# Kernel tuning notes

Measured on AMD Instinct MI355X. Metric: run time of the kernel, lower is better.

## Reference

```python
import jax, jax.numpy as jnp
import numpy as np

D_MODEL, D_STATE, D_CONV, EXPAND = 1024, 16, 4, 2
D_INNER = EXPAND * D_MODEL
BATCH, SEQ = 2, 2048


def setup_inputs() -> dict:
    key = jax.random.key(0)
    ks = jax.random.split(key, 10)
    s = lambda fan_in: 1.0 / np.sqrt(fan_in)
    return {
        "x": jax.random.normal(ks[0], (BATCH, SEQ, D_MODEL), jnp.float32),
        "W_in": jax.random.normal(ks[1], (2 * D_INNER, D_MODEL), jnp.float32) * s(D_MODEL),
        "w_conv": jax.random.normal(ks[2], (D_INNER, D_CONV), jnp.float32) * s(D_CONV),
        "b_conv": jax.random.normal(ks[3], (D_INNER,), jnp.float32) * 0.02,
        "W_x": jax.random.normal(ks[4], (D_INNER + 2 * D_STATE, D_INNER), jnp.float32) * s(D_INNER),
        "W_dt": jax.random.normal(ks[5], (D_INNER, D_INNER), jnp.float32) * s(D_INNER),
        "b_dt": jax.random.normal(ks[6], (D_INNER,), jnp.float32) * 0.02,
        "A_log": jnp.log(jax.random.uniform(ks[7], (D_INNER, D_STATE), jnp.float32, 1e-4, 1.0)),
        "D": jnp.ones((D_INNER,), jnp.float32),
        "W_out": jax.random.normal(ks[8], (D_MODEL, D_INNER), jnp.float32) * s(D_INNER),
    }


def _depthwise_causal_conv(x, w, b):
    # x: (B, L, C), w: (C, K), causal (left-pad K-1), matches conv1d(padding=K-1)[..., :L]
    K = w.shape[1]
    L = x.shape[1]
    xp = jnp.pad(x, ((0, 0), (K - 1, 0), (0, 0)))
    out = b
    for k in range(K):  # K is tiny (4)
        out = out + xp[:, k:k + L, :] * w[:, k]
    return out


def _selective_scan(x, delta, Bm, Cm, A, Dv):
    # x, delta: (B, L, d_inner); Bm, Cm: (B, L, d_state)
    def step(state, inp):
        x_t, d_t, B_t, C_t = inp  # (B,d_inner),(B,d_inner),(B,d_state),(B,d_state)
        decay = jnp.exp(d_t[..., None] * A)          # (B, d_inner, d_state)
        state = decay * state + B_t[:, None, :] * x_t[..., None]
        y_t = jnp.einsum('bds,bs->bd', state, C_t) + x_t * Dv
        return state, y_t

    init = jnp.zeros((x.shape[0], x.shape[2], A.shape[1]), x.dtype)
    xs = tuple(jnp.swapaxes(a, 0, 1) for a in (x, delta, Bm, Cm))
    _, ys = jax.lax.scan(step, init, xs)             # ys: (L, B, d_inner)
    return jnp.swapaxes(ys, 0, 1)


def reference(x, W_in, w_conv, b_conv, W_x, W_dt, b_dt, A_log, D, W_out):
    silu = jax.nn.silu
    xz = x @ W_in.T                                   # (B, L, 2*d_inner)
    x_inner, z = jnp.split(xz, 2, axis=-1)
    x_conv = silu(_depthwise_causal_conv(x_inner, w_conv, b_conv))
    x_dbl = x_conv @ W_x.T                            # (B, L, d_inner + 2*d_state)
    delta, Bm, Cm = jnp.split(x_dbl, [D_INNER, D_INNER + D_STATE], axis=-1)
    delta = jax.nn.softplus(delta @ W_dt.T + b_dt)
    A = -jnp.exp(A_log.astype(jnp.float32))
    y = _selective_scan(x_conv, delta, Bm, Cm, A, D)
    y = y * silu(z)
    return y @ W_out.T
```

## Files before the change

kernel.cpp:

```cpp
#include <hip/hip_runtime.h>
#include <hip/hip_bf16.h>


#define BATCH 2
#define SEQ   2048
#define DM    1024
#define DI    2048
#define DS    16
#define T_TOK (BATCH * SEQ)

#define CL 64
#define NC 32

typedef __bf16 v8bf __attribute__((ext_vector_type(8)));
typedef float  v4f  __attribute__((ext_vector_type(4)));

__device__ __forceinline__ void gld16(const void* g, void* l) {
    __builtin_amdgcn_global_load_lds(
        (const __attribute__((address_space(1))) void*)g,
        (__attribute__((address_space(3))) void*)l, 16, 0, 0);
}

__device__ __forceinline__ float b2f(__hip_bfloat16 v) { return __bfloat162float(v); }

__global__ void detect_dtype(const unsigned* __restrict__ Dptr, int* __restrict__ flag) {
    if (threadIdx.x == 0 && blockIdx.x == 0)
        *flag = (Dptr[0] == 0x3F803F80u) ? 1 : 0;
}

__device__ __forceinline__ float load_in(const void* p, size_t i, int isbf) {
    return isbf ? b2f(((const __hip_bfloat16*)p)[i]) : ((const float*)p)[i];
}

#define NBIG0 (T_TOK * DM)
#define NBIG1 (4096 * DM)
#define NBIG2 (DI * DI)
#define NBIG3 (DM * DI)
__global__ void convert_big(const void* __restrict__ s0, const void* __restrict__ s1,
                            const void* __restrict__ s2, const void* __restrict__ s3,
                            __hip_bfloat16* __restrict__ d0, __hip_bfloat16* __restrict__ d1,
                            __hip_bfloat16* __restrict__ d2, __hip_bfloat16* __restrict__ d3,
                            const int* __restrict__ flag) {
    if (*flag) return;
    size_t e = ((size_t)blockIdx.x * 256 + threadIdx.x) * 8;
    const float* src; __hip_bfloat16* dst;
    if (e < NBIG0)                      { src = (const float*)s0 + e;                 dst = d0 + e; }
    else if (e < NBIG0 + NBIG1)         { e -= NBIG0; src = (const float*)s1 + e;     dst = d1 + e; }
    else if (e < NBIG0 + NBIG1 + NBIG2) { e -= NBIG0 + NBIG1; src = (const float*)s2 + e; dst = d2 + e; }
    else                                { e -= NBIG0 + NBIG1 + NBIG2; src = (const float*)s3 + e; dst = d3 + e; }
    const float4 a = *(const float4*)src;
    const float4 b = *(const float4*)(src + 4);
    __bf16 o[8] = {(__bf16)a.x,(__bf16)a.y,(__bf16)a.z,(__bf16)a.w,
                   (__bf16)b.x,(__bf16)b.y,(__bf16)b.z,(__bf16)b.w};
    *(uint4*)dst = *(uint4*)&o[0];
}

__global__ void convert_small(const void* __restrict__ wconv, const void* __restrict__ bconv,
                              const void* __restrict__ bdt, const void* __restrict__ dv,
                              const void* __restrict__ A_log,
                              __hip_bfloat16* __restrict__ wconvb, __hip_bfloat16* __restrict__ bconvb,
                              __hip_bfloat16* __restrict__ bdtb, __hip_bfloat16* __restrict__ db,
                              float* __restrict__ Amat,
                              const int* __restrict__ flag) {
    const int isbf = *flag;
    const int i = blockIdx.x * 256 + threadIdx.x;
    if (i < 8192)        wconvb[i]        = __float2bfloat16(load_in(wconv, i, isbf));
    else if (i < 10240)  bconvb[i - 8192] = __float2bfloat16(load_in(bconv, i - 8192, isbf));
    else if (i < 12288)  bdtb[i - 10240]  = __float2bfloat16(load_in(bdt, i - 10240, isbf));
    else if (i < 14336)  db[i - 12288]    = __float2bfloat16(load_in(dv, i - 12288, isbf));
    else if (i < 47104)  Amat[i - 14336]  = -__expf(load_in(A_log, i - 14336, isbf));
}

__global__ __launch_bounds__(256) void transpose_wxd(
    const void* __restrict__ Wx, __hip_bfloat16* __restrict__ WxdT,
    const int* __restrict__ flag)
{
    const int isbf = *flag;
    __shared__ __bf16 t[64][72];
    const int bi = blockIdx.y * 64;
    const int bj = blockIdx.x * 64;
    const int rr = threadIdx.x >> 3;
    const int c0 = (threadIdx.x & 7) * 8;

#pragma unroll
    for (int k = 0; k < 2; k++) {
        const int r = rr + k * 32;
        const size_t src = (size_t)(bi + r) * DI + bj + c0;
        __bf16 o[8];
        if (isbf) {
            *(uint4*)&o[0] = *(const uint4*)((const __hip_bfloat16*)Wx + src);
        } else {
            const float* s = (const float*)Wx + src;
            const float4 a = *(const float4*)s;
            const float4 b = *(const float4*)(s + 4);
            o[0]=(__bf16)a.x; o[1]=(__bf16)a.y; o[2]=(__bf16)a.z; o[3]=(__bf16)a.w;
            o[4]=(__bf16)b.x; o[5]=(__bf16)b.y; o[6]=(__bf16)b.z; o[7]=(__bf16)b.w;
        }
        *(uint4*)&t[r][c0] = *(uint4*)&o[0];
    }
    __syncthreads();
#pragma unroll
    for (int k = 0; k < 2; k++) {
        const int dr = rr + k * 32;
        __bf16 o[8];
#pragma unroll
        for (int j = 0; j < 8; j++) o[j] = t[c0 + j][dr];
        *(uint4*)(WxdT + (size_t)(bj + dr) * DI + bi + c0) = *(uint4*)&o[0];
    }
}

__global__ void pad_bc(const void* __restrict__ Wx, __hip_bfloat16* __restrict__ Wxp,
                       const int* __restrict__ flag) {
    const int isbf = *flag;
    const size_t e = ((size_t)blockIdx.x * 256 + threadIdx.x) * 8;
    if (e >= (size_t)128 * DI) return;
    const size_t base = (size_t)2048 * DI;
    if (e >= (size_t)32 * DI) {
        __bf16 z[8] = {};
        *(uint4*)(Wxp + base + e) = *(uint4*)&z[0];
        return;
    }
    if (isbf) {
        *(uint4*)(Wxp + base + e) = *(const uint4*)((const __hip_bfloat16*)Wx + base + e);
    } else {
        const float* src = (const float*)Wx + base + e;
        const float4 a = *(const float4*)src;
        const float4 b = *(const float4*)(src + 4);
        __bf16 o[8] = {(__bf16)a.x,(__bf16)a.y,(__bf16)a.z,(__bf16)a.w,
                       (__bf16)b.x,(__bf16)b.y,(__bf16)b.z,(__bf16)b.w};
        *(uint4*)(Wxp + base + e) = *(uint4*)&o[0];
    }
}

template <int MODE, int TN>
__global__ __launch_bounds__(256) void gemm_bt(
    const __hip_bfloat16* __restrict__ Ac, const void* __restrict__ Araw,
    const __hip_bfloat16* __restrict__ Bc, const void* __restrict__ Braw,
    void* __restrict__ out0, void* __restrict__ out1,
    const __hip_bfloat16* __restrict__ bias,
    const int* __restrict__ flag,
    int M, int N, int K)
{
    constexpr int NF = TN / 32;
    constexpr int ASLOT = 512;
    constexpr int BSLOT = TN * 4;
    __shared__ v8bf Asv[2 * ASLOT];
    __shared__ v8bf Bsv[2 * BSLOT];

    const int isbf = *flag;
    const __hip_bfloat16* A  = (isbf && Araw) ? (const __hip_bfloat16*)Araw : Ac;
    const __hip_bfloat16* Bw = (isbf && Braw) ? (const __hip_bfloat16*)Braw : Bc;

    const int nx = gridDim.x;
    const int nblk = nx * gridDim.y;
    const int id = blockIdx.y * nx + blockIdx.x;
    const int sid = (id & 7) * (nblk >> 3) + (id >> 3);
    const int bxs = sid % nx;
    const int bys = sid / nx;

    const int tid  = threadIdx.x;
    const int bm   = bys * 128;
    const int bn   = bxs * TN;
    const int w    = tid >> 6;
    const int lane = tid & 63;
    const int wm   = (w >> 1) * 64;
    const int wn   = (w & 1) * (TN / 2);
    const int lrow  = lane & 15;
    const int lquad = lane >> 4;

    v4f acc[4][NF];
#pragma unroll
    for (int i = 0; i < 4; i++)
#pragma unroll
        for (int j = 0; j < NF; j++) acc[i][j] = (v4f){0.f, 0.f, 0.f, 0.f};

    const int r0 = tid >> 2;
    const int q0 = (tid & 3) ^ ((r0 >> 1) & 3);
    const __hip_bfloat16* gA0 = A  + (size_t)(bm + r0) * K + q0 * 8;
    const __hip_bfloat16* gA1 = A  + (size_t)(bm + 64 + r0) * K + q0 * 8;
    const __hip_bfloat16* gB0 = Bw + (size_t)(bn + r0) * K + q0 * 8;
    const __hip_bfloat16* gB1 = Bw + (size_t)(bn + 64 + r0) * K + q0 * 8;
    char* lA0 = (char*)Asv + tid * 16;
    char* lA1 = (char*)Asv + 4096 + tid * 16;
    char* lB0 = (char*)Bsv + tid * 16;
    char* lB1 = (char*)Bsv + 4096 + tid * 16;

    const int swz = lquad ^ ((lrow >> 1) & 3);
    int sA[4], sB[NF];
#pragma unroll
    for (int i = 0; i < 4; i++) sA[i] = (wm + i * 16 + lrow) * 4 + swz;
#pragma unroll
    for (int i = 0; i < NF; i++) sB[i] = (wn + i * 16 + lrow) * 4 + swz;

    const int NIT = K >> 5;
    gld16(gA0, lA0);
    gld16(gA1, lA1);
    gld16(gB0, lB0);
    if (TN == 128) gld16(gB1, lB1);

    int k = 32;
    for (int it = 0; it < NIT; ++it) {
        const int cb = it & 1;
        __syncthreads();
        if (it + 1 < NIT) {
            const int pa = (cb ^ 1) * 8192;
            const int pb = (cb ^ 1) * (BSLOT * 16);
            gld16(gA0 + k, lA0 + pa);
            gld16(gA1 + k, lA1 + pa);
            gld16(gB0 + k, lB0 + pb);
            if (TN == 128) gld16(gB1 + k, lB1 + pb);
            k += 32;
        }
        const int ca = cb * ASLOT;
        const int cbb = cb * BSLOT;
        v8bf af[4], bfr[NF];
#pragma unroll
        for (int i = 0; i < 4; i++)
            af[i] = Asv[ca + sA[i]];
#pragma unroll
        for (int i = 0; i < NF; i++)
            bfr[i] = Bsv[cbb + sB[i]];
#pragma unroll
        for (int mi = 0; mi < 4; mi++)
#pragma unroll
            for (int ni = 0; ni < NF; ni++)
                acc[mi][ni] = __builtin_amdgcn_mfma_f32_16x16x32_bf16(
                    af[mi], bfr[ni], acc[mi][ni], 0, 0, 0);
    }

#pragma unroll
    for (int mi = 0; mi < 4; mi++) {
#pragma unroll
        for (int ni = 0; ni < NF; ni++) {
#pragma unroll
            for (int r = 0; r < 4; r++) {
                const int grow = bm + wm + mi * 16 + lquad * 4 + r;
                const int gcol = bn + wn + ni * 16 + lrow;
                const float v = acc[mi][ni][r];
                if (MODE == 0) {
                    ((__hip_bfloat16*)out0)[(size_t)grow * N + gcol] = __float2bfloat16(v);
                } else if (MODE == 4) {
                    if (gcol < 2048) {
                        const float x = v + b2f(bias[gcol]);
                        const float sp = (x > 15.f) ? x : __logf(1.f + __expf(x));
                        ((__hip_bfloat16*)out0)[(size_t)grow * 2048 + gcol] = __float2bfloat16(sp);
                    } else if (gcol < 2080) {
                        ((float*)out1)[(size_t)grow * 32 + (gcol - 2048)] = v;
                    }
                } else {
                    if (isbf)
                        ((__hip_bfloat16*)out0)[(size_t)grow * N + gcol] = __float2bfloat16(v);
                    else
                        ((float*)out0)[(size_t)grow * N + gcol] = v;
                }
            }
        }
    }
}

__global__ __launch_bounds__(256) void conv_silu(
    const __hip_bfloat16* __restrict__ xz,
    const __hip_bfloat16* __restrict__ wconv,
    const __hip_bfloat16* __restrict__ bconv,
    __hip_bfloat16* __restrict__ xconv)
{
    const int idx = blockIdx.x * 256 + threadIdx.x;
    const int c8 = (idx & 255) << 3;
    const int tg = idx >> 8;
    const int tl = tg & (SEQ - 1);

    __bf16 wl[32], bl[8];
    *(uint4*)&wl[0]  = *(const uint4*)(wconv + c8 * 4);
    *(uint4*)&wl[8]  = *(const uint4*)(wconv + c8 * 4 + 8);
    *(uint4*)&wl[16] = *(const uint4*)(wconv + c8 * 4 + 16);
    *(uint4*)&wl[24] = *(const uint4*)(wconv + c8 * 4 + 24);
    *(uint4*)&bl[0]  = *(const uint4*)(bconv + c8);

    float acc[8];
#pragma unroll
    for (int cc = 0; cc < 8; cc++) acc[cc] = (float)bl[cc];

#pragma unroll
    for (int k = 0; k < 4; k++) {
        const int ts = tl - 3 + k;
        if (ts >= 0) {
            __bf16 xl[8];
            *(uint4*)&xl[0] = *(const uint4*)(xz + (size_t)(tg - 3 + k) * 4096 + c8);
#pragma unroll
            for (int cc = 0; cc < 8; cc++)
                acc[cc] += (float)wl[cc * 4 + k] * (float)xl[cc];
        }
    }

    __bf16 o[8];
#pragma unroll
    for (int cc = 0; cc < 8; cc++) {
        const float s = acc[cc] / (1.f + __expf(-acc[cc]));
        o[cc] = (__bf16)s;
    }
    *(uint4*)(xconv + (size_t)tg * DI + c8) = *(uint4*)&o[0];
}

__global__ __launch_bounds__(256) void scan_p1(
    const __hip_bfloat16* __restrict__ delta, const __hip_bfloat16* __restrict__ xconv,
    const float* __restrict__ BC, const float* __restrict__ Amat,
    float* __restrict__ Pws, float* __restrict__ Sws)
{
    const int d = blockIdx.x * 256 + threadIdx.x;
    const int c = blockIdx.y;
    const int b = blockIdx.z;
    const int tg0 = b * SEQ + c * CL;

    __shared__ float bc[CL * 32];
    for (int i = threadIdx.x; i < CL * 32; i += 256) bc[i] = BC[(size_t)tg0 * 32 + i];
    __syncthreads();

    float Areg[DS];
#pragma unroll
    for (int s = 0; s < DS; s++) Areg[s] = Amat[d * DS + s];

    float P[DS], S[DS];
#pragma unroll
    for (int s = 0; s < DS; s++) { P[s] = 1.f; S[s] = 0.f; }

    for (int i = 0; i < CL; i++) {
        const size_t tg = tg0 + i;
        const float dl = b2f(delta[tg * DI + d]);
        const float x  = b2f(xconv[tg * DI + d]);
#pragma unroll
        for (int s = 0; s < DS; s++) {
            const float e = __expf(dl * Areg[s]);
            P[s] *= e;
            S[s] = e * S[s] + bc[i * 32 + s] * x;
        }
    }

    const size_t base = (((size_t)b * NC + c) * DI + d) * DS;
#pragma unroll
    for (int s = 0; s < DS; s += 4) {
        *(float4*)(Pws + base + s) = make_float4(P[s], P[s+1], P[s+2], P[s+3]);
        *(float4*)(Sws + base + s) = make_float4(S[s], S[s+1], S[s+2], S[s+3]);
    }
}

__global__ void scan_p2(float* __restrict__ Pws, float* __restrict__ Sws) {
    const int idx = blockIdx.x * 256 + threadIdx.x;
    const int b  = idx >> 15;
    const int ds = idx & 32767;
    float carry = 0.f;
    for (int c = 0; c < NC; c++) {
        const size_t a = (((size_t)b * NC + c) << 15) + ds;
        const float p  = Pws[a];
        const float sv = Sws[a];
        Sws[a] = carry;
        carry = p * carry + sv;
    }
}

__global__ __launch_bounds__(256) void scan_p3(
    const __hip_bfloat16* __restrict__ delta, const __hip_bfloat16* __restrict__ xconv,
    const float* __restrict__ BC, const float* __restrict__ Amat,
    const float* __restrict__ Sws, const __hip_bfloat16* __restrict__ xz,
    const __hip_bfloat16* __restrict__ Dv, __hip_bfloat16* __restrict__ yg)
{
    const int d = blockIdx.x * 256 + threadIdx.x;
    const int c = blockIdx.y;
    const int b = blockIdx.z;
    const int tg0 = b * SEQ + c * CL;

    __shared__ float bc[CL * 32];
    for (int i = threadIdx.x; i < CL * 32; i += 256) bc[i] = BC[(size_t)tg0 * 32 + i];
    __syncthreads();

    float Areg[DS];
#pragma unroll
    for (int s = 0; s < DS; s++) Areg[s] = Amat[d * DS + s];

    const size_t base = (((size_t)b * NC + c) * DI + d) * DS;
    float S[DS];
#pragma unroll
    for (int s = 0; s < DS; s += 4) {
        const float4 v = *(const float4*)(Sws + base + s);
        S[s] = v.x; S[s+1] = v.y; S[s+2] = v.z; S[s+3] = v.w;
    }
    const float Dd = b2f(Dv[d]);

    for (int i = 0; i < CL; i++) {
        const size_t tg = tg0 + i;
        const float dl = b2f(delta[tg * DI + d]);
        const float x  = b2f(xconv[tg * DI + d]);
        float y = 0.f;
#pragma unroll
        for (int s = 0; s < DS; s++) {
            const float e = __expf(dl * Areg[s]);
            S[s] = e * S[s] + bc[i * 32 + s] * x;
            y += S[s] * bc[i * 32 + 16 + s];
        }
        y += x * Dd;
        const float z = b2f(xz[tg * 4096 + 2048 + d]);
        const float g = z / (1.f + __expf(-z));
        yg[tg * DI + d] = __float2bfloat16(y * g);
    }
}

extern "C" void kernel_launch(void* const* d_in, const int* in_sizes, int n_in,
                              void* d_out, int out_size, void* d_ws, size_t ws_size,
                              hipStream_t stream)
{
    const void* x_raw     = d_in[0];
    const void* W_in_raw  = d_in[1];
    const void* wconv_raw = d_in[2];
    const void* bconv_raw = d_in[3];
    const void* W_x_raw   = d_in[4];
    const void* W_dt_raw  = d_in[5];
    const void* b_dt_raw  = d_in[6];
    const void* A_log_raw = d_in[7];
    const void* D_raw     = d_in[8];
    const void* W_out_raw = d_in[9];

    char* ws = (char*)d_ws;
    size_t off = 0;
    auto alloc = [&](size_t bytes) { char* p = ws + off; off += (bytes + 255) & ~(size_t)255; return p; };
    int*            FLAG  = (int*)alloc(256);
    __hip_bfloat16* XB    = (__hip_bfloat16*)alloc((size_t)T_TOK * DM * 2);
    __hip_bfloat16* WINB  = (__hip_bfloat16*)alloc((size_t)4096 * DM * 2);
    __hip_bfloat16* WDTB  = (__hip_bfloat16*)alloc((size_t)DI * DI * 2);
    __hip_bfloat16* WOUTB = (__hip_bfloat16*)alloc((size_t)DM * DI * 2);
    __hip_bfloat16* WCONVB= (__hip_bfloat16*)alloc((size_t)DI * 4 * 2);
    __hip_bfloat16* BCONVB= (__hip_bfloat16*)alloc((size_t)DI * 2);
    __hip_bfloat16* BDTB  = (__hip_bfloat16*)alloc((size_t)DI * 2);
    __hip_bfloat16* DB    = (__hip_bfloat16*)alloc((size_t)DI * 2);
    __hip_bfloat16* XZ    = (__hip_bfloat16*)alloc((size_t)T_TOK * 4096 * 2);
    __hip_bfloat16* XCONV = (__hip_bfloat16*)alloc((size_t)T_TOK * DI * 2);
    __hip_bfloat16* WXDT  = (__hip_bfloat16*)alloc((size_t)DI * DI * 2);
    __hip_bfloat16* WXPAD = (__hip_bfloat16*)alloc((size_t)2176 * DI * 2);
    float*          BC    = (float*)alloc((size_t)T_TOK * 32 * 4);
    __hip_bfloat16* DELTA = (__hip_bfloat16*)alloc((size_t)T_TOK * DI * 2);
    float*          AMAT  = (float*)alloc((size_t)DI * DS * 4);
    float*          PWS   = (float*)alloc((size_t)BATCH * NC * DI * DS * 4);
    float*          SWS   = (float*)alloc((size_t)BATCH * NC * DI * DS * 4);
    __hip_bfloat16* YG    = (__hip_bfloat16*)alloc((size_t)T_TOK * DI * 2);

    detect_dtype<<<1, 64, 0, stream>>>((const unsigned*)D_raw, FLAG);
    convert_big<<<(NBIG0 + NBIG1 + NBIG2 + NBIG3) / (256 * 8), 256, 0, stream>>>(
        x_raw, W_in_raw, W_dt_raw, W_out_raw, XB, WINB, WDTB, WOUTB, FLAG);
    convert_small<<<184, 256, 0, stream>>>(wconv_raw, bconv_raw, b_dt_raw, D_raw, A_log_raw,
                                           WCONVB, BCONVB, BDTB, DB, AMAT, FLAG);
    transpose_wxd<<<dim3(32, 32), 256, 0, stream>>>(W_x_raw, WXDT, FLAG);

    gemm_bt<0, 128><<<dim3(16, 16), 256, 0, stream>>>(
        WDTB, W_dt_raw, WXDT, nullptr, WXPAD, nullptr, nullptr, FLAG, DI, DI, DI);

    pad_bc<<<128, 256, 0, stream>>>(W_x_raw, WXPAD, FLAG);

    gemm_bt<0, 128><<<dim3(32, 32), 256, 0, stream>>>(
        XB, x_raw, WINB, W_in_raw, XZ, nullptr, nullptr, FLAG, T_TOK, 4096, DM);

    conv_silu<<<T_TOK, 256, 0, stream>>>(XZ, WCONVB, BCONVB, XCONV);

    gemm_bt<4, 128><<<dim3(17, 32), 256, 0, stream>>>(
        XCONV, nullptr, WXPAD, nullptr, DELTA, BC, BDTB, FLAG, T_TOK, 2176, DI);

    scan_p1<<<dim3(DI / 256, NC, BATCH), 256, 0, stream>>>(DELTA, XCONV, BC, AMAT, PWS, SWS);
    scan_p2<<<(BATCH * DI * DS) / 256, 256, 0, stream>>>(PWS, SWS);
    scan_p3<<<dim3(DI / 256, NC, BATCH), 256, 0, stream>>>(DELTA, XCONV, BC, AMAT, SWS, XZ, DB, YG);

    gemm_bt<3, 64><<<dim3(16, 32), 256, 0, stream>>>(
        YG, nullptr, WOUTB, W_out_raw, d_out, nullptr, nullptr, FLAG, T_TOK, DM, DI);
}
```

Baseline: 468.6 us.

## Merge prep kernels, fuse dual GEMMs, grid-barrier scan, move softplus into scan

```diff
diff --git a/kernel.cpp b/kernel.cpp
--- a/kernel.cpp
+++ b/kernel.cpp
@@ -23,9 +23,8 @@
 
 __device__ __forceinline__ float b2f(__hip_bfloat16 v) { return __bfloat162float(v); }
 
-__global__ void detect_dtype(const unsigned* __restrict__ Dptr, int* __restrict__ flag) {
-    if (threadIdx.x == 0 && blockIdx.x == 0)
-        *flag = (Dptr[0] == 0x3F803F80u) ? 1 : 0;
+__device__ __forceinline__ int is_bf(const void* Dref) {
+    return ((const unsigned*)Dref)[0] == 0x3F803F80u;
 }
 
 __device__ __forceinline__ float load_in(const void* p, size_t i, int isbf) {
@@ -36,110 +35,110 @@
 #define NBIG1 (4096 * DM)
 #define NBIG2 (DI * DI)
 #define NBIG3 (DM * DI)
-__global__ void convert_big(const void* __restrict__ s0, const void* __restrict__ s1,
-                            const void* __restrict__ s2, const void* __restrict__ s3,
-                            __hip_bfloat16* __restrict__ d0, __hip_bfloat16* __restrict__ d1,
-                            __hip_bfloat16* __restrict__ d2, __hip_bfloat16* __restrict__ d3,
-                            const int* __restrict__ flag) {
-    if (*flag) return;
-    size_t e = ((size_t)blockIdx.x * 256 + threadIdx.x) * 8;
-    const float* src; __hip_bfloat16* dst;
-    if (e < NBIG0)                      { src = (const float*)s0 + e;                 dst = d0 + e; }
-    else if (e < NBIG0 + NBIG1)         { e -= NBIG0; src = (const float*)s1 + e;     dst = d1 + e; }
-    else if (e < NBIG0 + NBIG1 + NBIG2) { e -= NBIG0 + NBIG1; src = (const float*)s2 + e; dst = d2 + e; }
-    else                                { e -= NBIG0 + NBIG1 + NBIG2; src = (const float*)s3 + e; dst = d3 + e; }
-    const float4 a = *(const float4*)src;
-    const float4 b = *(const float4*)(src + 4);
-    __bf16 o[8] = {(__bf16)a.x,(__bf16)a.y,(__bf16)a.z,(__bf16)a.w,
-                   (__bf16)b.x,(__bf16)b.y,(__bf16)b.z,(__bf16)b.w};
-    *(uint4*)dst = *(uint4*)&o[0];
-}
-
-__global__ void convert_small(const void* __restrict__ wconv, const void* __restrict__ bconv,
-                              const void* __restrict__ bdt, const void* __restrict__ dv,
-                              const void* __restrict__ A_log,
-                              __hip_bfloat16* __restrict__ wconvb, __hip_bfloat16* __restrict__ bconvb,
-                              __hip_bfloat16* __restrict__ bdtb, __hip_bfloat16* __restrict__ db,
-                              float* __restrict__ Amat,
-                              const int* __restrict__ flag) {
-    const int isbf = *flag;
-    const int i = blockIdx.x * 256 + threadIdx.x;
-    if (i < 8192)        wconvb[i]        = __float2bfloat16(load_in(wconv, i, isbf));
-    else if (i < 10240)  bconvb[i - 8192] = __float2bfloat16(load_in(bconv, i - 8192, isbf));
-    else if (i < 12288)  bdtb[i - 10240]  = __float2bfloat16(load_in(bdt, i - 10240, isbf));
-    else if (i < 14336)  db[i - 12288]    = __float2bfloat16(load_in(dv, i - 12288, isbf));
-    else if (i < 47104)  Amat[i - 14336]  = -__expf(load_in(A_log, i - 14336, isbf));
-}
-
-__global__ __launch_bounds__(256) void transpose_wxd(
+#define NB_BIG 7168
+#define NB_TR  1024
+#define NB_SM  184
+#define NB_PAD 128
+#define NB_ALL (NB_BIG + NB_TR + NB_SM + NB_PAD)
+
+__global__ __launch_bounds__(256) void convert_all(
+    const void* __restrict__ s0, const void* __restrict__ s1,
+    const void* __restrict__ s2, const void* __restrict__ s3,
+    __hip_bfloat16* __restrict__ d0, __hip_bfloat16* __restrict__ d1,
+    __hip_bfloat16* __restrict__ d2, __hip_bfloat16* __restrict__ d3,
+    const void* __restrict__ wconv, const void* __restrict__ bconv,
+    const void* __restrict__ bdt, const void* __restrict__ dv,
+    const void* __restrict__ A_log,
+    __hip_bfloat16* __restrict__ wconvb, __hip_bfloat16* __restrict__ bconvb,
+    __hip_bfloat16* __restrict__ bdtb, __hip_bfloat16* __restrict__ db,
+    float* __restrict__ Amat,
     const void* __restrict__ Wx, __hip_bfloat16* __restrict__ WxdT,
-    const int* __restrict__ flag)
-{
-    const int isbf = *flag;
+    __hip_bfloat16* __restrict__ Wxp,
+    unsigned* __restrict__ bar)
+{
     __shared__ __bf16 t[64][72];
-    const int bi = blockIdx.y * 64;
-    const int bj = blockIdx.x * 64;
-    const int rr = threadIdx.x >> 3;
-    const int c0 = (threadIdx.x & 7) * 8;
-
-#pragma unroll
-    for (int k = 0; k < 2; k++) {
-        const int r = rr + k * 32;
-        const size_t src = (size_t)(bi + r) * DI + bj + c0;
-        __bf16 o[8];
-        if (isbf) {
-            *(uint4*)&o[0] = *(const uint4*)((const __hip_bfloat16*)Wx + src);
-        } else {
-            const float* s = (const float*)Wx + src;
-            const float4 a = *(const float4*)s;
-            const float4 b = *(const float4*)(s + 4);
-            o[0]=(__bf16)a.x; o[1]=(__bf16)a.y; o[2]=(__bf16)a.z; o[3]=(__bf16)a.w;
-            o[4]=(__bf16)b.x; o[5]=(__bf16)b.y; o[6]=(__bf16)b.z; o[7]=(__bf16)b.w;
-        }
-        *(uint4*)&t[r][c0] = *(uint4*)&o[0];
-    }
-    __syncthreads();
-#pragma unroll
-    for (int k = 0; k < 2; k++) {
-        const int dr = rr + k * 32;
-        __bf16 o[8];
-#pragma unroll
-        for (int j = 0; j < 8; j++) o[j] = t[c0 + j][dr];
-        *(uint4*)(WxdT + (size_t)(bj + dr) * DI + bi + c0) = *(uint4*)&o[0];
-    }
-}
-
-__global__ void pad_bc(const void* __restrict__ Wx, __hip_bfloat16* __restrict__ Wxp,
-                       const int* __restrict__ flag) {
-    const int isbf = *flag;
-    const size_t e = ((size_t)blockIdx.x * 256 + threadIdx.x) * 8;
-    if (e >= (size_t)128 * DI) return;
-    const size_t base = (size_t)2048 * DI;
-    if (e >= (size_t)32 * DI) {
-        __bf16 z[8] = {};
-        *(uint4*)(Wxp + base + e) = *(uint4*)&z[0];
-        return;
-    }
-    if (isbf) {
-        *(uint4*)(Wxp + base + e) = *(const uint4*)((const __hip_bfloat16*)Wx + base + e);
-    } else {
-        const float* src = (const float*)Wx + base + e;
+    const int isbf = is_bf(dv);
+    const int bid = blockIdx.x;
+
+    if (bid < NB_BIG) {
+        if (isbf) return;
+        size_t e = ((size_t)bid * 256 + threadIdx.x) * 8;
+        const float* src; __hip_bfloat16* dst;
+        if (e < NBIG0)                      { src = (const float*)s0 + e;                 dst = d0 + e; }
+        else if (e < NBIG0 + NBIG1)         { e -= NBIG0; src = (const float*)s1 + e;     dst = d1 + e; }
+        else if (e < NBIG0 + NBIG1 + NBIG2) { e -= NBIG0 + NBIG1; src = (const float*)s2 + e; dst = d2 + e; }
+        else                                { e -= NBIG0 + NBIG1 + NBIG2; src = (const float*)s3 + e; dst = d3 + e; }
         const float4 a = *(const float4*)src;
         const float4 b = *(const float4*)(src + 4);
         __bf16 o[8] = {(__bf16)a.x,(__bf16)a.y,(__bf16)a.z,(__bf16)a.w,
                        (__bf16)b.x,(__bf16)b.y,(__bf16)b.z,(__bf16)b.w};
-        *(uint4*)(Wxp + base + e) = *(uint4*)&o[0];
+        *(uint4*)dst = *(uint4*)&o[0];
+    } else if (bid < NB_BIG + NB_TR) {
+        const int b2 = bid - NB_BIG;
+        const int bi = (b2 >> 5) * 64;
+        const int bj = (b2 & 31) * 64;
+        const int rr = threadIdx.x >> 3;
+        const int c0 = (threadIdx.x & 7) * 8;
+#pragma unroll
+        for (int k = 0; k < 2; k++) {
+            const int r = rr + k * 32;
+            const size_t src = (size_t)(bi + r) * DI + bj + c0;
+            __bf16 o[8];
+            if (isbf) {
+                *(uint4*)&o[0] = *(const uint4*)((const __hip_bfloat16*)Wx + src);
+            } else {
+                const float* s = (const float*)Wx + src;
+                const float4 a = *(const float4*)s;
+                const float4 b = *(const float4*)(s + 4);
+                o[0]=(__bf16)a.x; o[1]=(__bf16)a.y; o[2]=(__bf16)a.z; o[3]=(__bf16)a.w;
+                o[4]=(__bf16)b.x; o[5]=(__bf16)b.y; o[6]=(__bf16)b.z; o[7]=(__bf16)b.w;
+            }
+            *(uint4*)&t[r][c0] = *(uint4*)&o[0];
+        }
+        __syncthreads();
+#pragma unroll
+        for (int k = 0; k < 2; k++) {
+            const int dr = rr + k * 32;
+            __bf16 o[8];
+#pragma unroll
+            for (int j = 0; j < 8; j++) o[j] = t[c0 + j][dr];
+            *(uint4*)(WxdT + (size_t)(bj + dr) * DI + bi + c0) = *(uint4*)&o[0];
+        }
+    } else if (bid < NB_BIG + NB_TR + NB_SM) {
+        if (bid == NB_BIG + NB_TR && threadIdx.x == 0) *bar = 0u;
+        const int i = (bid - (NB_BIG + NB_TR)) * 256 + threadIdx.x;
+        if (i < 8192)        wconvb[i]        = __float2bfloat16(load_in(wconv, i, isbf));
+        else if (i < 10240)  bconvb[i - 8192] = __float2bfloat16(load_in(bconv, i - 8192, isbf));
+        else if (i < 12288)  bdtb[i - 10240]  = __float2bfloat16(load_in(bdt, i - 10240, isbf));
+        else if (i < 14336)  db[i - 12288]    = __float2bfloat16(load_in(dv, i - 12288, isbf));
+        else if (i < 47104)  Amat[i - 14336]  = -__expf(load_in(A_log, i - 14336, isbf));
+    } else {
+        const size_t e = ((size_t)(bid - (NB_BIG + NB_TR + NB_SM)) * 256 + threadIdx.x) * 8;
+        if (e >= (size_t)128 * DI) return;
+        const size_t base = (size_t)2048 * DI;
+        if (e >= (size_t)32 * DI) {
+            __bf16 z[8] = {};
+            *(uint4*)(Wxp + base + e) = *(uint4*)&z[0];
+            return;
+        }
+        if (isbf) {
+            *(uint4*)(Wxp + base + e) = *(const uint4*)((const __hip_bfloat16*)Wx + base + e);
+        } else {
+            const float* src = (const float*)Wx + base + e;
+            const float4 a = *(const float4*)src;
+            const float4 b = *(const float4*)(src + 4);
+            __bf16 o[8] = {(__bf16)a.x,(__bf16)a.y,(__bf16)a.z,(__bf16)a.w,
+                           (__bf16)b.x,(__bf16)b.y,(__bf16)b.z,(__bf16)b.w};
+            *(uint4*)(Wxp + base + e) = *(uint4*)&o[0];
+        }
     }
 }
 
 template <int MODE, int TN>
-__global__ __launch_bounds__(256) void gemm_bt(
-    const __hip_bfloat16* __restrict__ Ac, const void* __restrict__ Araw,
-    const __hip_bfloat16* __restrict__ Bc, const void* __restrict__ Braw,
+__device__ __forceinline__ void gemm_core(
+    const __hip_bfloat16* __restrict__ A, const __hip_bfloat16* __restrict__ Bw,
     void* __restrict__ out0, void* __restrict__ out1,
-    const __hip_bfloat16* __restrict__ bias,
-    const int* __restrict__ flag,
-    int M, int N, int K)
+    int isbf, int id, int nx, int nblk, int N, int K)
 {
     constexpr int NF = TN / 32;
     constexpr int ASLOT = 512;
@@ -147,13 +146,6 @@
     __shared__ v8bf Asv[2 * ASLOT];
     __shared__ v8bf Bsv[2 * BSLOT];
 
-    const int isbf = *flag;
-    const __hip_bfloat16* A  = (isbf && Araw) ? (const __hip_bfloat16*)Araw : Ac;
-    const __hip_bfloat16* Bw = (isbf && Braw) ? (const __hip_bfloat16*)Braw : Bc;
-
-    const int nx = gridDim.x;
-    const int nblk = nx * gridDim.y;
-    const int id = blockIdx.y * nx + blockIdx.x;
     const int sid = (id & 7) * (nblk >> 3) + (id >> 3);
     const int bxs = sid % nx;
     const int bys = sid / nx;
@@ -239,11 +231,9 @@
                 const float v = acc[mi][ni][r];
                 if (MODE == 0) {
                     ((__hip_bfloat16*)out0)[(size_t)grow * N + gcol] = __float2bfloat16(v);
-                } else if (MODE == 4) {
+                } else if (MODE == 1) {
                     if (gcol < 2048) {
-                        const float x = v + b2f(bias[gcol]);
-                        const float sp = (x > 15.f) ? x : __logf(1.f + __expf(x));
-                        ((__hip_bfloat16*)out0)[(size_t)grow * 2048 + gcol] = __float2bfloat16(sp);
+                        ((__hip_bfloat16*)out0)[(size_t)grow * 2048 + gcol] = __float2bfloat16(v);
                     } else if (gcol < 2080) {
                         ((float*)out1)[(size_t)grow * 32 + (gcol - 2048)] = v;
                     }
@@ -258,6 +248,42 @@
     }
 }
 
+template <int MODE, int TN>
+__global__ __launch_bounds__(256) void gemm_single(
+    const __hip_bfloat16* __restrict__ Ac, const void* __restrict__ Araw,
+    const __hip_bfloat16* __restrict__ Bc, const void* __restrict__ Braw,
+    void* __restrict__ out0, void* __restrict__ out1,
+    const void* __restrict__ Dref, int N, int K)
+{
+    const int isbf = is_bf(Dref);
+    const __hip_bfloat16* A = (isbf && Araw) ? (const __hip_bfloat16*)Araw : Ac;
+    const __hip_bfloat16* B = (isbf && Braw) ? (const __hip_bfloat16*)Braw : Bc;
+    const int nx = gridDim.x;
+    const int nblk = gridDim.x * gridDim.y;
+    const int id = blockIdx.y * nx + blockIdx.x;
+    gemm_core<MODE, TN>(A, B, out0, out1, isbf, id, nx, nblk, N, K);
+}
+
+__global__ __launch_bounds__(256) void gemm_dual(
+    const __hip_bfloat16* __restrict__ A1c, const void* __restrict__ A1raw,
+    const __hip_bfloat16* __restrict__ B1c, const void* __restrict__ B1raw,
+    void* __restrict__ o1,
+    const __hip_bfloat16* __restrict__ A2c, const void* __restrict__ A2raw,
+    const __hip_bfloat16* __restrict__ B2,
+    void* __restrict__ o2,
+    const void* __restrict__ Dref)
+{
+    const int isbf = is_bf(Dref);
+    if (blockIdx.x < 1024) {
+        const __hip_bfloat16* A = (isbf && A1raw) ? (const __hip_bfloat16*)A1raw : A1c;
+        const __hip_bfloat16* B = (isbf && B1raw) ? (const __hip_bfloat16*)B1raw : B1c;
+        gemm_core<0, 128>(A, B, o1, nullptr, isbf, blockIdx.x, 32, 1024, 4096, 1024);
+    } else {
+        const __hip_bfloat16* A = (isbf && A2raw) ? (const __hip_bfloat16*)A2raw : A2c;
+        gemm_core<0, 128>(A, B2, o2, nullptr, isbf, blockIdx.x - 1024, 16, 256, 2048, 2048);
+    }
+}
+
 __global__ __launch_bounds__(256) void conv_silu(
     const __hip_bfloat16* __restrict__ xz,
     const __hip_bfloat16* __restrict__ wconv,
@@ -301,10 +327,31 @@
     *(uint4*)(xconv + (size_t)tg * DI + c8) = *(uint4*)&o[0];
 }
 
-__global__ __launch_bounds__(256) void scan_p1(
-    const __hip_bfloat16* __restrict__ delta, const __hip_bfloat16* __restrict__ xconv,
-    const float* __restrict__ BC, const float* __restrict__ Amat,
-    float* __restrict__ Pws, float* __restrict__ Sws)
+#define SCAN_NBLK (8 * NC * BATCH)
+
+__device__ __forceinline__ void gbar(unsigned* bar, unsigned target) {
+    __threadfence();
+    __syncthreads();
+    if (threadIdx.x == 0) {
+        __hip_atomic_fetch_add(bar, 1u, __ATOMIC_ACQ_REL, __HIP_MEMORY_SCOPE_AGENT);
+        while (__hip_atomic_load(bar, __ATOMIC_ACQUIRE, __HIP_MEMORY_SCOPE_AGENT) < target)
+            __builtin_amdgcn_s_sleep(16);
+    }
+    __syncthreads();
+    __threadfence();
+}
+
+__device__ __forceinline__ float softplus_f(float x) {
+    return (x > 15.f) ? x : __logf(1.f + __expf(x));
+}
+
+__global__ __launch_bounds__(256) void scan_all(
+    const __hip_bfloat16* __restrict__ dlin, const __hip_bfloat16* __restrict__ xconv,
+    const float* __restrict__ BCg, const float* __restrict__ Amat,
+    const __hip_bfloat16* __restrict__ bdt,
+    float* __restrict__ Pws, float* __restrict__ Sws,
+    const __hip_bfloat16* __restrict__ xz, const __hip_bfloat16* __restrict__ Dv,
+    __hip_bfloat16* __restrict__ yg, unsigned* __restrict__ bar)
 {
     const int d = blockIdx.x * 256 + threadIdx.x;
     const int c = blockIdx.y;
@@ -312,12 +359,13 @@
     const int tg0 = b * SEQ + c * CL;
 
     __shared__ float bc[CL * 32];
-    for (int i = threadIdx.x; i < CL * 32; i += 256) bc[i] = BC[(size_t)tg0 * 32 + i];
+    for (int i = threadIdx.x; i < CL * 32; i += 256) bc[i] = BCg[(size_t)tg0 * 32 + i];
     __syncthreads();
 
     float Areg[DS];
 #pragma unroll
     for (int s = 0; s < DS; s++) Areg[s] = Amat[d * DS + s];
+    const float bd = b2f(bdt[d]);
 
     float P[DS], S[DS];
 #pragma unroll
@@ -325,7 +373,7 @@
 
     for (int i = 0; i < CL; i++) {
         const size_t tg = tg0 + i;
-        const float dl = b2f(delta[tg * DI + d]);
+        const float dl = softplus_f(b2f(dlin[tg * DI + d]) + bd);
         const float x  = b2f(xconv[tg * DI + d]);
 #pragma unroll
         for (int s = 0; s < DS; s++) {
@@ -341,60 +389,45 @@
         *(float4*)(Pws + base + s) = make_float4(P[s], P[s+1], P[s+2], P[s+3]);
         *(float4*)(Sws + base + s) = make_float4(S[s], S[s+1], S[s+2], S[s+3]);
     }
-}
-
-__global__ void scan_p2(float* __restrict__ Pws, float* __restrict__ Sws) {
-    const int idx = blockIdx.x * 256 + threadIdx.x;
-    const int b  = idx >> 15;
-    const int ds = idx & 32767;
-    float carry = 0.f;
-    for (int c = 0; c < NC; c++) {
-        const size_t a = (((size_t)b * NC + c) << 15) + ds;
-        const float p  = Pws[a];
-        const float sv = Sws[a];
-        Sws[a] = carry;
-        carry = p * carry + sv;
-    }
-}
-
-__global__ __launch_bounds__(256) void scan_p3(
-    const __hip_bfloat16* __restrict__ delta, const __hip_bfloat16* __restrict__ xconv,
-    const float* __restrict__ BC, const float* __restrict__ Amat,
-    const float* __restrict__ Sws, const __hip_bfloat16* __restrict__ xz,
-    const __hip_bfloat16* __restrict__ Dv, __hip_bfloat16* __restrict__ yg)
-{
-    const int d = blockIdx.x * 256 + threadIdx.x;
-    const int c = blockIdx.y;
-    const int b = blockIdx.z;
-    const int tg0 = b * SEQ + c * CL;
-
-    __shared__ float bc[CL * 32];
-    for (int i = threadIdx.x; i < CL * 32; i += 256) bc[i] = BC[(size_t)tg0 * 32 + i];
-    __syncthreads();
-
-    float Areg[DS];
-#pragma unroll
-    for (int s = 0; s < DS; s++) Areg[s] = Amat[d * DS + s];
-
-    const size_t base = (((size_t)b * NC + c) * DI + d) * DS;
-    float S[DS];
+
+    gbar(bar, SCAN_NBLK);
+
+    {
+        const int fid = ((blockIdx.z * NC + blockIdx.y) * 8 + blockIdx.x) * 256 + threadIdx.x;
+        if (fid < BATCH * DI * DS) {
+            const int bb = fid >> 15;
+            const int ds = fid & 32767;
+            float carry = 0.f;
+            for (int c2 = 0; c2 < NC; c2++) {
+                const size_t a = (((size_t)bb * NC + c2) << 15) + ds;
+                const float p  = Pws[a];
+                const float sv = Sws[a];
+                Sws[a] = carry;
+                carry = p * carry + sv;
+            }
+        }
+    }
+
+    gbar(bar, 2 * SCAN_NBLK);
+
+    float S3[DS];
 #pragma unroll
     for (int s = 0; s < DS; s += 4) {
         const float4 v = *(const float4*)(Sws + base + s);
-        S[s] = v.x; S[s+1] = v.y; S[s+2] = v.z; S[s+3] = v.w;
+        S3[s] = v.x; S3[s+1] = v.y; S3[s+2] = v.z; S3[s+3] = v.w;
     }
     const float Dd = b2f(Dv[d]);
 
     for (int i = 0; i < CL; i++) {
         const size_t tg = tg0 + i;
-        const float dl = b2f(delta[tg * DI + d]);
+        const float dl = softplus_f(b2f(dlin[tg * DI + d]) + bd);
         const float x  = b2f(xconv[tg * DI + d]);
         float y = 0.f;
 #pragma unroll
         for (int s = 0; s < DS; s++) {
             const float e = __expf(dl * Areg[s]);
-            S[s] = e * S[s] + bc[i * 32 + s] * x;
-            y += S[s] * bc[i * 32 + 16 + s];
+            S3[s] = e * S3[s] + bc[i * 32 + s] * x;
+            y += S3[s] * bc[i * 32 + 16 + s];
         }
         y += x * Dd;
         const float z = b2f(xz[tg * 4096 + 2048 + d]);
@@ -421,7 +454,7 @@
     char* ws = (char*)d_ws;
     size_t off = 0;
     auto alloc = [&](size_t bytes) { char* p = ws + off; off += (bytes + 255) & ~(size_t)255; return p; };
-    int*            FLAG  = (int*)alloc(256);
+    unsigned*       BAR   = (unsigned*)alloc(256);
     __hip_bfloat16* XB    = (__hip_bfloat16*)alloc((size_t)T_TOK * DM * 2);
     __hip_bfloat16* WINB  = (__hip_bfloat16*)alloc((size_t)4096 * DM * 2);
     __hip_bfloat16* WDTB  = (__hip_bfloat16*)alloc((size_t)DI * DI * 2);
@@ -441,30 +474,24 @@
     float*          SWS   = (float*)alloc((size_t)BATCH * NC * DI * DS * 4);
     __hip_bfloat16* YG    = (__hip_bfloat16*)alloc((size_t)T_TOK * DI * 2);
 
-    detect_dtype<<<1, 64, 0, stream>>>((const unsigned*)D_raw, FLAG);
-    convert_big<<<(NBIG0 + NBIG1 + NBIG2 + NBIG3) / (256 * 8), 256, 0, stream>>>(
-        x_raw, W_in_raw, W_dt_raw, W_out_raw, XB, WINB, WDTB, WOUTB, FLAG);
-    convert_small<<<184, 256, 0, stream>>>(wconv_raw, bconv_raw, b_dt_raw, D_raw, A_log_raw,
-                                           WCONVB, BCONVB, BDTB, DB, AMAT, FLAG);
-    transpose_wxd<<<dim3(32, 32), 256, 0, stream>>>(W_x_raw, WXDT, FLAG);
-
-    gemm_bt<0, 128><<<dim3(16, 16), 256, 0, stream>>>(
-        WDTB, W_dt_raw, WXDT, nullptr, WXPAD, nullptr, nullptr, FLAG, DI, DI, DI);
-
-    pad_bc<<<128, 256, 0, stream>>>(W_x_raw, WXPAD, FLAG);
-
-    gemm_bt<0, 128><<<dim3(32, 32), 256, 0, stream>>>(
-        XB, x_raw, WINB, W_in_raw, XZ, nullptr, nullptr, FLAG, T_TOK, 4096, DM);
+    convert_all<<<NB_ALL, 256, 0, stream>>>(
+        x_raw, W_in_raw, W_dt_raw, W_out_raw, XB, WINB, WDTB, WOUTB,
+        wconv_raw, bconv_raw, b_dt_raw, D_raw, A_log_raw,
+        WCONVB, BCONVB, BDTB, DB, AMAT,
+        W_x_raw, WXDT, WXPAD, BAR);
+
+    gemm_dual<<<1280, 256, 0, stream>>>(
+        XB, x_raw, WINB, W_in_raw, XZ,
+        WDTB, W_dt_raw, WXDT, WXPAD, D_raw);
 
     conv_silu<<<T_TOK, 256, 0, stream>>>(XZ, WCONVB, BCONVB, XCONV);
 
-    gemm_bt<4, 128><<<dim3(17, 32), 256, 0, stream>>>(
-        XCONV, nullptr, WXPAD, nullptr, DELTA, BC, BDTB, FLAG, T_TOK, 2176, DI);
-
-    scan_p1<<<dim3(DI / 256, NC, BATCH), 256, 0, stream>>>(DELTA, XCONV, BC, AMAT, PWS, SWS);
-    scan_p2<<<(BATCH * DI * DS) / 256, 256, 0, stream>>>(PWS, SWS);
-    scan_p3<<<dim3(DI / 256, NC, BATCH), 256, 0, stream>>>(DELTA, XCONV, BC, AMAT, SWS, XZ, DB, YG);
-
-    gemm_bt<3, 64><<<dim3(16, 32), 256, 0, stream>>>(
-        YG, nullptr, WOUTB, W_out_raw, d_out, nullptr, nullptr, FLAG, T_TOK, DM, DI);
-}
+    gemm_single<1, 128><<<dim3(17, 32), 256, 0, stream>>>(
+        XCONV, nullptr, WXPAD, nullptr, DELTA, BC, D_raw, 2176, 2048);
+
+    scan_all<<<dim3(DI / 256, NC, BATCH), 256, 0, stream>>>(
+        DELTA, XCONV, BC, AMAT, BDTB, PWS, SWS, XZ, DB, YG, BAR);
+
+    gemm_single<3, 128><<<dim3(8, 32), 256, 0, stream>>>(
+        YG, nullptr, WOUTB, W_out_raw, d_out, nullptr, D_raw, 1024, 2048);
+}
```

After: 760.1 us. 1.62x slower.
